# Optimization experiments

Measured on AMD Instinct MI355X. Metric: run time of the kernel, lower is better.

Reference implementation:

```python
import jax, jax.numpy as jnp
import numpy as np

NEG_SLOPE = 0.2  # PyG GATConv default negative_slope


def gat_conv(x, edge_index, W, att_src, att_dst, bias):
    # PyG GATConv, heads=1, add_self_loops=True, lin bias=False, final bias added
    N = x.shape[0]
    h = x @ W                                     # [N, F]
    loops = jnp.arange(N, dtype=edge_index.dtype)
    src = jnp.concatenate([edge_index[0], loops])
    dst = jnp.concatenate([edge_index[1], loops])
    a_src = h @ att_src                           # [N]
    a_dst = h @ att_dst                           # [N]
    e = a_src[src] + a_dst[dst]
    e = jnp.where(e > 0, e, NEG_SLOPE * e)        # leaky_relu
    m = jax.ops.segment_max(e, dst, num_segments=N)
    w = jnp.exp(e - m[dst])
    denom = jax.ops.segment_sum(w, dst, num_segments=N)
    alpha = w / denom[dst]
    out = jax.ops.segment_sum(h[src] * alpha[:, None], dst, num_segments=N)
    return out + bias


def gcn_conv(x, edge_index, W, b):
    # PyG GCNConv: add self-loops + symmetric normalization
    N = x.shape[0]
    loops = jnp.arange(N, dtype=edge_index.dtype)
    src = jnp.concatenate([edge_index[0], loops])
    dst = jnp.concatenate([edge_index[1], loops])
    deg = jax.ops.segment_sum(jnp.ones(src.shape[0], dtype=x.dtype), dst, num_segments=N)
    dinv = jax.lax.rsqrt(jnp.maximum(deg, 1e-12))  # deg >= 1 thanks to self-loops
    norm = dinv[src] * dinv[dst]
    xw = x @ W
    return jax.ops.segment_sum(xw[src] * norm[:, None], dst, num_segments=N) + b


def get_final_node(x, batch, num_graphs):
    nn_ = jax.ops.segment_sum(jnp.ones(x.shape[0], dtype=jnp.int32), batch, num_segments=num_graphs)
    cum = jnp.concatenate([jnp.zeros(1, dtype=nn_.dtype), jnp.cumsum(nn_)[:-1]])
    return x[cum]


def ontology_emb(table, e1, e2, W, asrc, adst, b, idx_map):
    emb = gat_conv(table, e1, W, asrc, adst, b)
    emb = gat_conv(emb, e2, W, asrc, adst, b)
    return emb[idx_map]


def _forward(spec_emb, diag_table, proce_table, atc_table,
             diag_W, diag_asrc, diag_adst, diag_b,
             proce_W, proce_asrc, proce_adst, proce_b,
             atc_W, atc_asrc, atc_adst, atc_b,
             gcn_W1, gcn_b1, gcn_W2, gcn_b2, gcn_W3, gcn_b3,
             diag_e1, diag_e2, proce_e1, proce_e2, atc_e1, atc_e2,
             diag_map, proce_map, atc_map,
             left_x, left_graph_index, right_x, right_graph_index,
             left_x_batch, right_x_batch, num_graphs):
    diag_emb = ontology_emb(diag_table, diag_e1, diag_e2, diag_W, diag_asrc, diag_adst, diag_b, diag_map)
    proce_emb = ontology_emb(proce_table, proce_e1, proce_e2, proce_W, proce_asrc, proce_adst, proce_b, proce_map)
    atc_emb = ontology_emb(atc_table, atc_e1, atc_e2, atc_W, atc_asrc, atc_adst, atc_b, atc_map)
    all_emb = jnp.concatenate([spec_emb, diag_emb, proce_emb, atc_emb], axis=0)
    lh = all_emb[left_x[:, 0]]   # squeeze(dim=1)
    rh = all_emb[right_x[:, 0]]
    for W, b in ((gcn_W1, gcn_b1), (gcn_W2, gcn_b2), (gcn_W3, gcn_b3)):
        lh = gcn_conv(lh, left_graph_index, W, b)
        rh = gcn_conv(rh, right_graph_index, W, b)
    lf = get_final_node(lh, left_x_batch, num_graphs)
    rf = get_final_node(rh, right_x_batch, num_graphs)
    eps = 1e-6  # CosineSimilarity eps
    num = jnp.sum(lf * rf, axis=-1)
    den = jnp.maximum(jnp.linalg.norm(lf, axis=-1), eps) * jnp.maximum(jnp.linalg.norm(rf, axis=-1), eps)
    return num / den


def setup_inputs() -> dict:
    key = jax.random.key(0)
    ks = jax.random.split(key, 32)
    HID = 128
    B, NPG = 2048, 50
    N = B * NPG               # 102400 nodes per side
    E_PAT = 409600            # 4 edges per node
    DIAG_N, DIAG_L = 30000, 20000
    PROCE_N, PROCE_L = 12000, 8000
    ATC_N, ATC_L = 6000, 4000
    ALL = 1 + DIAG_L + PROCE_L + ATC_L
    f = lambda k, s: jax.random.normal(k, s, dtype=jnp.float32)
    scale = 0.1
    inp = {
        'spec_emb': f(ks[0], (1, HID)),
        'diag_table': f(ks[1], (DIAG_N, HID)),
        'proce_table': f(ks[2], (PROCE_N, HID)),
        'atc_table': f(ks[3], (ATC_N, HID)),
    }
    for i, nm in enumerate(['diag', 'proce', 'atc']):
        inp[nm + '_W'] = f(ks[4 + i], (HID, HID)) * scale
        inp[nm + '_asrc'] = f(ks[7 + i], (HID,)) * scale
        inp[nm + '_adst'] = f(ks[10 + i], (HID,)) * scale
        inp[nm + '_b'] = jnp.zeros((HID,), jnp.float32)
    for j in range(3):
        inp['gcn_W%d' % (j + 1)] = f(ks[13 + j], (HID, HID)) * scale
        inp['gcn_b%d' % (j + 1)] = jnp.zeros((HID,), jnp.float32)
    inp['diag_e1'] = jax.random.randint(ks[16], (2, DIAG_N), 0, DIAG_N, dtype=jnp.int32)
    inp['diag_e2'] = jax.random.randint(ks[17], (2, DIAG_N), 0, DIAG_N, dtype=jnp.int32)
    inp['proce_e1'] = jax.random.randint(ks[18], (2, PROCE_N), 0, PROCE_N, dtype=jnp.int32)
    inp['proce_e2'] = jax.random.randint(ks[19], (2, PROCE_N), 0, PROCE_N, dtype=jnp.int32)
    inp['atc_e1'] = jax.random.randint(ks[20], (2, ATC_N), 0, ATC_N, dtype=jnp.int32)
    inp['atc_e2'] = jax.random.randint(ks[21], (2, ATC_N), 0, ATC_N, dtype=jnp.int32)
    inp['diag_map'] = jnp.arange(DIAG_L, dtype=jnp.int32)
    inp['proce_map'] = jnp.arange(PROCE_L, dtype=jnp.int32)
    inp['atc_map'] = jnp.arange(ATC_L, dtype=jnp.int32)
    inp['left_x'] = jax.random.randint(ks[22], (N, 1), 0, ALL, dtype=jnp.int32)
    inp['right_x'] = jax.random.randint(ks[23], (N, 1), 0, ALL, dtype=jnp.int32)
    inp['left_graph_index'] = jax.random.randint(ks[24], (2, E_PAT), 0, N, dtype=jnp.int32)
    inp['right_graph_index'] = jax.random.randint(ks[25], (2, E_PAT), 0, N, dtype=jnp.int32)
    batch = jnp.repeat(jnp.arange(B, dtype=jnp.int32), NPG)
    inp['left_x_batch'] = batch
    inp['right_x_batch'] = batch
    inp['num_graphs'] = B
    return inp


def reference(spec_emb, diag_table, proce_table, atc_table,
              diag_W, diag_asrc, diag_adst, diag_b,
              proce_W, proce_asrc, proce_adst, proce_b,
              atc_W, atc_asrc, atc_adst, atc_b,
              gcn_W1, gcn_b1, gcn_W2, gcn_b2, gcn_W3, gcn_b3,
              diag_e1, diag_e2, proce_e1, proce_e2, atc_e1, atc_e2,
              diag_map, proce_map, atc_map,
              left_x, left_graph_index, right_x, right_graph_index,
              left_x_batch, right_x_batch, num_graphs):
    return _forward(spec_emb, diag_table, proce_table, atc_table,
                    diag_W, diag_asrc, diag_adst, diag_b,
                    proce_W, proce_asrc, proce_adst, proce_b,
                    atc_W, atc_asrc, atc_adst, atc_b,
                    gcn_W1, gcn_b1, gcn_W2, gcn_b2, gcn_W3, gcn_b3,
                    diag_e1, diag_e2, proce_e1, proce_e2, atc_e1, atc_e2,
                    diag_map, proce_map, atc_map,
                    left_x, left_graph_index, right_x, right_graph_index,
                    left_x_batch, right_x_batch, num_graphs)
```

## Files before the change

### kernel.cpp

```cpp
#include <hip/hip_runtime.h>
#include <hip/hip_bf16.h>

#define HID 128

typedef unsigned int uint;
typedef unsigned short ushort;
typedef short short8 __attribute__((ext_vector_type(8)));
typedef float f32x4 __attribute__((ext_vector_type(4)));

static inline int cdiv_i(long a, long b) { return (int)((a + b - 1) / b); }
static inline int imax_i(int a, int b) { return a > b ? a : b; }

__device__ __forceinline__ float bf2f(uint hi) {
    return __builtin_bit_cast(float, hi << 16);
}
__device__ __forceinline__ ushort f2bf(float f) {
    uint u = __builtin_bit_cast(uint, f);
    u = (u + 0x7fffu + ((u >> 16) & 1u)) >> 16;
    return (ushort)u;
}

struct CsrDesc {
    const int* esrc[8];
    const int* edst[8];
    int ebase[9];
    int nbase[9];
    int totE;
};

template <typename AT>
__device__ __forceinline__ void load_afrag(const AT* __restrict__ A, long row,
                                           int koff, short8& af) {
    if constexpr (__is_same(AT, ushort)) {
        const uint4 raw = *(const uint4*)(A + row * 128 + koff);
        af = __builtin_bit_cast(short8, raw);
    } else {
        const float4* p = (const float4*)(A + row * 128 + koff);
        const float4 x0 = p[0], x1 = p[1];
        af[0] = (short)f2bf(x0.x); af[1] = (short)f2bf(x0.y);
        af[2] = (short)f2bf(x0.z); af[3] = (short)f2bf(x0.w);
        af[4] = (short)f2bf(x1.x); af[5] = (short)f2bf(x1.y);
        af[6] = (short)f2bf(x1.z); af[7] = (short)f2bf(x1.w);
    }
}

struct GOnto {
    const ushort* Wt0; const ushort* Wt1; const ushort* Wt2;
    const float* s0; const float* s1; const float* s2;
    const float* d0; const float* d1; const float* d2;
    int bs1, bs2;
    int r1, r2, r3;
};

template <typename AT>
__device__ void gemm_onto_dev(int b, const AT* __restrict__ x0,
                              const AT* __restrict__ x1, const AT* __restrict__ x2,
                              const GOnto& g, ushort* __restrict__ H,
                              float* __restrict__ as_o, float* __restrict__ ad_o) {
    const int gid = (b >= g.bs1) + (b >= g.bs2);
    const ushort* Wt = (gid == 0) ? g.Wt0 : (gid == 1) ? g.Wt1 : g.Wt2;
    const float* avs = (gid == 0) ? g.s0 : (gid == 1) ? g.s1 : g.s2;
    const float* avd = (gid == 0) ? g.d0 : (gid == 1) ? g.d1 : g.d2;
    const AT* Ag = (gid == 0) ? x0 : (gid == 1) ? x1 : x2;
    const int bloc = b - ((gid == 0) ? 0 : (gid == 1) ? g.bs1 : g.bs2);
    const long rb = (gid == 0) ? 0 : (gid == 1) ? g.r1 : g.r2;
    const long Mg = ((gid == 0) ? g.r1 : (gid == 1) ? g.r2 : g.r3) - rb;

    const int tid = threadIdx.x;
    const int wave = tid >> 6, lane = tid & 63;
    const int r = lane & 15, q = lane >> 4;
    const long m0 = (long)bloc * 128 + wave * 32;

    f32x4 acc[2][8];
#pragma unroll
    for (int mi = 0; mi < 2; ++mi)
#pragma unroll
        for (int ni = 0; ni < 8; ++ni) acc[mi][ni] = (f32x4)0.f;

#pragma unroll
    for (int t = 0; t < 4; ++t) {
        const int koff = t * 32 + q * 8;
        short8 bfr[8];
#pragma unroll
        for (int ni = 0; ni < 8; ++ni) {
            const uint4 raw = *(const uint4*)(Wt + (ni * 16 + r) * 128 + koff);
            bfr[ni] = __builtin_bit_cast(short8, raw);
        }
#pragma unroll
        for (int mi = 0; mi < 2; ++mi) {
            long row = m0 + mi * 16 + r;
            if (row >= Mg) row = Mg - 1;
            short8 af;
            load_afrag<AT>(Ag, row, koff, af);
#pragma unroll
            for (int ni = 0; ni < 8; ++ni)
                acc[mi][ni] = __builtin_amdgcn_mfma_f32_16x16x32_bf16(
                    af, bfr[ni], acc[mi][ni], 0, 0, 0);
        }
    }

    ushort* Hg = H + rb * 128;
#pragma unroll
    for (int mi = 0; mi < 2; ++mi) {
#pragma unroll
        for (int ni = 0; ni < 8; ++ni) {
            const int col = ni * 16 + r;
#pragma unroll
            for (int reg = 0; reg < 4; ++reg) {
                const long row = m0 + mi * 16 + q * 4 + reg;
                if (row < Mg) Hg[row * 128 + col] = f2bf(acc[mi][ni][reg]);
            }
        }
    }

    float asv[8], adv[8];
#pragma unroll
    for (int ni = 0; ni < 8; ++ni) {
        asv[ni] = avs[ni * 16 + r];
        adv[ni] = avd[ni * 16 + r];
    }
#pragma unroll
    for (int mi = 0; mi < 2; ++mi) {
#pragma unroll
        for (int reg = 0; reg < 4; ++reg) {
            float ps = 0.f, pd = 0.f;
#pragma unroll
            for (int ni = 0; ni < 8; ++ni) {
                ps += acc[mi][ni][reg] * asv[ni];
                pd += acc[mi][ni][reg] * adv[ni];
            }
#pragma unroll
            for (int o = 1; o < 16; o <<= 1) {
                ps += __shfl_xor(ps, o);
                pd += __shfl_xor(pd, o);
            }
            const long row = m0 + mi * 16 + q * 4 + reg;
            if (r == 0 && row < Mg) {
                as_o[rb + row] = ps;
                ad_o[rb + row] = pd;
            }
        }
    }
}

__global__ __launch_bounds__(256) void gemm_onto_l2(const ushort* __restrict__ x0,
                                                    const ushort* __restrict__ x1,
                                                    const ushort* __restrict__ x2,
                                                    GOnto g, ushort* __restrict__ H,
                                                    float* __restrict__ as_o,
                                                    float* __restrict__ ad_o) {
    gemm_onto_dev<ushort>(blockIdx.x, x0, x1, x2, g, H, as_o, ad_o);
}

struct EmbSrc {
    const float* spec; const ushort* oE;
    const int* m0; const int* m1; const int* m2;
    int lb2, lb3, r1, r2;
};

__device__ __forceinline__ short8 load_emb(const EmbSrc& e, long row, int koff) {
    short8 af;
    if (row == 0) {
        const float4* pp = (const float4*)(e.spec + koff);
        const float4 x0 = pp[0], x1 = pp[1];
        af[0] = (short)f2bf(x0.x); af[1] = (short)f2bf(x0.y);
        af[2] = (short)f2bf(x0.z); af[3] = (short)f2bf(x0.w);
        af[4] = (short)f2bf(x1.x); af[5] = (short)f2bf(x1.y);
        af[6] = (short)f2bf(x1.z); af[7] = (short)f2bf(x1.w);
        return af;
    }
    const int r = (int)row;
    const int seg = (r >= e.lb2) + (r >= e.lb3);
    const int local = r - ((seg == 0) ? 1 : (seg == 1) ? e.lb2 : e.lb3);
    const int* mp = (seg == 0) ? e.m0 : (seg == 1) ? e.m1 : e.m2;
    const int rb = (seg == 0) ? 0 : (seg == 1) ? e.r1 : e.r2;
    const long sr = (long)rb + mp[local];
    return __builtin_bit_cast(short8, *(const uint4*)(e.oE + sr * 128 + koff));
}

__device__ void gemm_pat_tile(const EmbSrc& es, const ushort* __restrict__ Wt,
                              ushort* __restrict__ C, long m0blk, long rowEnd) {
    const int tid = threadIdx.x;
    const int wave = tid >> 6, lane = tid & 63;
    const int r = lane & 15, q = lane >> 4;
    const long m0 = m0blk + wave * 32;

    f32x4 acc[2][8];
#pragma unroll
    for (int mi = 0; mi < 2; ++mi)
#pragma unroll
        for (int ni = 0; ni < 8; ++ni) acc[mi][ni] = (f32x4)0.f;

#pragma unroll
    for (int t = 0; t < 4; ++t) {
        const int koff = t * 32 + q * 8;
        short8 bfr[8];
#pragma unroll
        for (int ni = 0; ni < 8; ++ni) {
            const uint4 raw = *(const uint4*)(Wt + (ni * 16 + r) * 128 + koff);
            bfr[ni] = __builtin_bit_cast(short8, raw);
        }
#pragma unroll
        for (int mi = 0; mi < 2; ++mi) {
            long row = m0 + mi * 16 + r;
            if (row >= rowEnd) row = rowEnd - 1;
            const short8 af = load_emb(es, row, koff);
#pragma unroll
            for (int ni = 0; ni < 8; ++ni)
                acc[mi][ni] = __builtin_amdgcn_mfma_f32_16x16x32_bf16(
                    af, bfr[ni], acc[mi][ni], 0, 0, 0);
        }
    }

#pragma unroll
    for (int mi = 0; mi < 2; ++mi) {
#pragma unroll
        for (int ni = 0; ni < 8; ++ni) {
            const int col = ni * 16 + r;
#pragma unroll
            for (int reg = 0; reg < 4; ++reg) {
                const long row = m0 + mi * 16 + q * 4 + reg;
                if (row < rowEnd) C[row * 128 + col] = f2bf(acc[mi][ni][reg]);
            }
        }
    }
}

__global__ __launch_bounds__(256) void gemm_pat(EmbSrc es,
                                                const ushort* __restrict__ Wt,
                                                ushort* __restrict__ C, int M) {
    const long m0 = (long)blockIdx.x * 256;
    gemm_pat_tile(es, Wt, C, m0, M);
    if (m0 + 128 < M) gemm_pat_tile(es, Wt, C, m0 + 128, M);
}

__device__ __forceinline__ void fold1_dev(int idx, const float* __restrict__ W2,
                                          const float* __restrict__ b2,
                                          const float* __restrict__ W3,
                                          float* __restrict__ W23b) {
    if (idx >= 129 * 128) return;
    const int i = idx >> 7, j = idx & 127;
    const float* a = (i < 128) ? (W2 + i * 128) : b2;
    float s = 0.f;
#pragma unroll 8
    for (int k = 0; k < 128; ++k) s += a[k] * W3[k * 128 + j];
    W23b[idx] = s;
}

__device__ __forceinline__ void fold2_dev(int idx, const float* __restrict__ W1,
                                          const float* __restrict__ b1,
                                          const float* __restrict__ W23b,
                                          ushort* __restrict__ WpT,
                                          float* __restrict__ cbuf) {
    if (idx >= 130 * 128) return;
    const int i = idx >> 7, j = idx & 127;
    if (i == 129) { cbuf[128 + j] = W23b[128 * 128 + j]; return; }
    const float* a = (i < 128) ? (W1 + i * 128) : b1;
    float s = 0.f;
#pragma unroll 8
    for (int k = 0; k < 128; ++k) s += a[k] * W23b[k * 128 + j];
    if (i < 128) WpT[j * 128 + i] = f2bf(s);
    else cbuf[j] = s;
}

__device__ __forceinline__ void mark_dev(int i, const int* __restrict__ lEg,
                                         const int* __restrict__ rEg, int EP,
                                         int NP, int* __restrict__ mk,
                                         int testBit, int setBit) {
    int src, dst;
    if (i < 2 * EP) {
        const int side = i >= EP;
        const int e = i - side * EP;
        const int* eg = side ? rEg : lEg;
        src = side * NP + eg[e];
        dst = side * NP + eg[EP + e];
    } else if (i < 2 * EP + 2 * NP) {
        src = dst = i - 2 * EP;
    } else return;
    if (mk[dst] & testBit) {
        const int old = mk[src];
        if (!(old & setBit)) mk[src] = old | setBit;
    }
}

__device__ __forceinline__ void csr_count_dev(int i, const CsrDesc& d,
                                              int* __restrict__ cnt) {
    if (i >= d.totE) return;
    int li = 0;
#pragma unroll
    for (int k = 1; k < 8; ++k) li += (i >= d.ebase[k]);
    const int v = d.nbase[li] + d.edst[li][i - d.ebase[li]];
    atomicAdd(&cnt[v], 1);
}

struct PackPrep {
    const float* W2; const float* b2; const float* W3; float* W23b;
    const float* wsrc[3]; ushort* wt_out;
    int* cnt; int NV;
    const int* bL; const int* bR; int NP;
    int* gfL; int* gfR; int* mk;
    int nbF1, nbWT, nbInit;
};

__global__ __launch_bounds__(256) void k_prep(PackPrep p) {
    const int b = blockIdx.x, tid = threadIdx.x;
    if (b < p.nbF1) {
        fold1_dev(b * 256 + tid, p.W2, p.b2, p.W3, p.W23b);
    } else if (b < p.nbF1 + p.nbWT) {
        const int idx = (b - p.nbF1) * 256 + tid;
        if (idx < 3 * 16384) {
            const int m = idx >> 14;
            const int e = idx & 16383;
            const int n = e >> 7, k = e & 127;
            p.wt_out[idx] = f2bf(p.wsrc[m][k * 128 + n]);
        }
    } else {
        const int i = (b - p.nbF1 - p.nbWT) * 256 + tid;
        if (i < p.NV) p.cnt[i] = 0;
        if (i < 2 * p.NP) {
            const int side = i >= p.NP;
            const int ii = i - (side ? p.NP : 0);
            const int* bb = side ? p.bR : p.bL;
            int* gf = side ? p.gfR : p.gfL;
            const int cur = bb[ii];
            const int prev = (ii == 0) ? -1 : bb[ii - 1];
            int m = 0;
            if (cur > prev) {
                for (int g = prev + 1; g <= cur; ++g) gf[g] = ii;
                m = 1;
            }
            p.mk[i] = m;
        }
    }
}

struct PackBig {
    const float* x0; const float* x1; const float* x2;
    GOnto go; ushort* H; float* as_o; float* ad_o;
    const float* W1; const float* b1; const float* W23b;
    ushort* WpT; float* cbuf;
    CsrDesc dsc; int* cnt;
    const int* lEg; const int* rEg; int EP; int NP; int* mk;
    int nbGemm, nbF2, nbCnt;
};

__global__ __launch_bounds__(256) void k_big1(PackBig p) {
    const int b = blockIdx.x, tid = threadIdx.x;
    if (b < p.nbGemm) {
        gemm_onto_dev<float>(b, p.x0, p.x1, p.x2, p.go, p.H, p.as_o, p.ad_o);
    } else if (b < p.nbGemm + p.nbF2) {
        fold2_dev((b - p.nbGemm) * 256 + tid, p.W1, p.b1, p.W23b, p.WpT, p.cbuf);
    } else if (b < p.nbGemm + p.nbF2 + p.nbCnt) {
        csr_count_dev((b - p.nbGemm - p.nbF2) * 256 + tid, p.dsc, p.cnt);
    } else {
        mark_dev((b - p.nbGemm - p.nbF2 - p.nbCnt) * 256 + tid, p.lEg, p.rEg,
                 p.EP, p.NP, p.mk, 1, 2);
    }
}

__device__ void scan_tile_dev(const int* __restrict__ in, int* __restrict__ out,
                              int* __restrict__ bsum, int n, int pn0, int pcnt,
                              float* __restrict__ dinv, int tb, int tid,
                              int* sbuf) {
    const int base = tb * 1024 + tid * 4;
    int v[4];
    int s = 0;
#pragma unroll
    for (int k = 0; k < 4; ++k) {
        const int i = base + k;
        v[k] = (i < n) ? (in[i] + 1) : 0;
        if (i >= pn0 && i < pn0 + pcnt)
            dinv[i - pn0] = rsqrtf(fmaxf((float)v[k], 1e-12f));
        s += v[k];
    }
    sbuf[tid] = s;
    __syncthreads();
    int x = s;
    for (int o = 1; o < 256; o <<= 1) {
        const int t = (tid >= o) ? sbuf[tid - o] : 0;
        __syncthreads();
        x += t;
        sbuf[tid] = x;
        __syncthreads();
    }
    int run = x - s;
#pragma unroll
    for (int k = 0; k < 4; ++k) {
        const int i = base + k;
        if (i < n) out[i] = run;
        run += v[k];
    }
    if (tid == 255) bsum[tb] = x;
}

struct PackScan {
    const int* cnt; int* offs; int* bsum;
    int NV; int pn0; int pcnt; float* dinv;
    const int* lEg; const int* rEg; int EP; int NP; int* mk;
    int nbScan;
};

__global__ __launch_bounds__(256) void k_scan(PackScan p) {
    __shared__ int sbuf[256];
    const int b = blockIdx.x, tid = threadIdx.x;
    if (b < p.nbScan) {
        scan_tile_dev(p.cnt, p.offs, p.bsum, p.NV, p.pn0, p.pcnt, p.dinv, b,
                      tid, sbuf);
    } else {
        mark_dev((b - p.nbScan) * 256 + tid, p.lEg, p.rEg, p.EP, p.NP, p.mk,
                 2, 4);
    }
}

__global__ __launch_bounds__(256) void k_scanfin(int* __restrict__ out,
                                                 int* __restrict__ out2,
                                                 const int* __restrict__ bsum,
                                                 int n, int nbData) {
    __shared__ int sbuf[256];
    const int tb = blockIdx.x, tid = threadIdx.x;
    int pLim = tb < nbData ? tb : nbData;
    int pth = 0;
    for (int j = tid; j < pLim; j += 256) pth += bsum[j];
    sbuf[tid] = pth;
    __syncthreads();
    for (int o = 128; o > 0; o >>= 1) {
        if (tid < o) sbuf[tid] += sbuf[tid + o];
        __syncthreads();
    }
    const int prefix = sbuf[0];
    const int base = tb * 1024 + tid * 4;
#pragma unroll
    for (int k = 0; k < 4; ++k) {
        const int i = base + k;
        if (i < n) {
            const int v = out[i] + prefix;
            out[i] = v;
            out2[i] = v;
        } else if (i == n) {
            out[i] = prefix + ((tb < nbData) ? bsum[tb] : 0);
        }
    }
}

struct FillP {
    CsrDesc dsc;
    const int* offs; int* offs2; const int* cnt;
    int* srcl; int4* pedge; const float* dinv;
    const int* lx; const int* rx; const int* mk;
    int NP, pB;
    int eStart, eCount, vStart, vCount;
};

__device__ void fill_dev(const FillP& f, int idx) {
    if (idx < f.eCount) {
        const int i = f.eStart + idx;
        int li = 0;
#pragma unroll
        for (int k = 1; k < 8; ++k) li += (i >= f.dsc.ebase[k]);
        const int j = i - f.dsc.ebase[li];
        const int v = f.dsc.nbase[li] + f.dsc.edst[li][j];
        const int s = f.dsc.esrc[li][j];
        if (li >= 6) {
            const int n2l = v - f.dsc.nbase[6];
            if (f.mk[n2l] == 0) return;
            const int sg = (li - 6) * f.NP + s;
            const int cidx = atomicAdd(&f.offs2[v], 1);
            int4 rec;
            rec.x = sg;
            rec.y = (li == 7 ? f.rx : f.lx)[s];
            rec.z = __float_as_int(f.dinv[n2l] * f.dinv[sg]);
            rec.w = 0;
            f.pedge[cidx - f.pB] = rec;
        } else {
            const int cidx = atomicAdd(&f.offs2[v], 1);
            f.srcl[cidx] = s;
        }
    } else if (idx < f.eCount + f.vCount) {
        const int v = f.vStart + (idx - f.eCount);
        int li = 0;
#pragma unroll
        for (int k = 1; k < 8; ++k) li += (v >= f.dsc.nbase[k]);
        const int s = v - f.dsc.nbase[li];
        if (li >= 6) {
            const int n2l = v - f.dsc.nbase[6];
            if (f.mk[n2l] == 0) return;
            const int cidx = f.offs[v] + f.cnt[v];
            const int sg = (li - 6) * f.NP + s;
            int4 rec;
            rec.x = sg;
            rec.y = (li == 7 ? f.rx : f.lx)[s];
            rec.z = __float_as_int(f.dinv[n2l] * f.dinv[sg]);
            rec.w = 0;
            f.pedge[cidx - f.pB] = rec;
        } else {
            f.srcl[f.offs[v] + f.cnt[v]] = s;
        }
    }
}

__global__ __launch_bounds__(256) void k_fill(FillP f) {
    fill_dev(f, blockIdx.x * 256 + threadIdx.x);
}

struct GatP {
    int r1, r2;
    int ob0, ob1, ob2;
    const float* b0; const float* b1; const float* b2;
};

__device__ __forceinline__ void acc8(float* acc, float w, const uint4 v) {
    acc[0] += w * bf2f(v.x & 0xffff);
    acc[1] += w * bf2f(v.x >> 16);
    acc[2] += w * bf2f(v.y & 0xffff);
    acc[3] += w * bf2f(v.y >> 16);
    acc[4] += w * bf2f(v.z & 0xffff);
    acc[5] += w * bf2f(v.z >> 16);
    acc[6] += w * bf2f(v.w & 0xffff);
    acc[7] += w * bf2f(v.w >> 16);
}

__device__ void gat_dev(int node, int ql, const ushort* __restrict__ h,
                        const float* __restrict__ as, const float* __restrict__ ad,
                        const int* __restrict__ offs, const int* __restrict__ srcl,
                        const GatP& p, ushort* __restrict__ out, int Mtot) {
    if (node >= Mtot) return;
    const int gid = (node >= p.r1) + (node >= p.r2);
    const int rb = (gid == 0) ? 0 : (gid == 1) ? p.r1 : p.r2;
    const int ob = (gid == 0) ? p.ob0 : (gid == 1) ? p.ob1 : p.ob2;
    const float* bias = (gid == 0) ? p.b0 : (gid == 1) ? p.b1 : p.b2;
    const int local = node - rb;
    const int beg = offs[ob + local], end = offs[ob + local + 1];
    const float adv = ad[node];
    float denom = 0.f;
    float acc[8] = {0.f, 0.f, 0.f, 0.f, 0.f, 0.f, 0.f, 0.f};
    int j = beg;
    for (; j + 2 <= end; j += 2) {
        const int s0 = srcl[j], s1 = srcl[j + 1];
        float e0 = as[rb + s0] + adv; e0 = (e0 > 0.f) ? e0 : 0.2f * e0;
        float e1 = as[rb + s1] + adv; e1 = (e1 > 0.f) ? e1 : 0.2f * e1;
        const float w0 = __expf(e0), w1 = __expf(e1);
        const uint4 v0 = *(const uint4*)(h + (size_t)(rb + s0) * 128 + ql * 8);
        const uint4 v1 = *(const uint4*)(h + (size_t)(rb + s1) * 128 + ql * 8);
        denom += w0 + w1;
        acc8(acc, w0, v0);
        acc8(acc, w1, v1);
    }
    if (j < end) {
        const int s0 = srcl[j];
        float e0 = as[rb + s0] + adv; e0 = (e0 > 0.f) ? e0 : 0.2f * e0;
        const float w0 = __expf(e0);
        const uint4 v0 = *(const uint4*)(h + (size_t)(rb + s0) * 128 + ql * 8);
        denom += w0;
        acc8(acc, w0, v0);
    }
    const float inv = 1.f / denom;
    const float4 bv0 = *(const float4*)(bias + ql * 8);
    const float4 bv1 = *(const float4*)(bias + ql * 8 + 4);
    uint4 o;
    o.x = (uint)f2bf(acc[0] * inv + bv0.x) | ((uint)f2bf(acc[1] * inv + bv0.y) << 16);
    o.y = (uint)f2bf(acc[2] * inv + bv0.z) | ((uint)f2bf(acc[3] * inv + bv0.w) << 16);
    o.z = (uint)f2bf(acc[4] * inv + bv1.x) | ((uint)f2bf(acc[5] * inv + bv1.y) << 16);
    o.w = (uint)f2bf(acc[6] * inv + bv1.z) | ((uint)f2bf(acc[7] * inv + bv1.w) << 16);
    *(uint4*)(out + (size_t)node * 128 + ql * 8) = o;
}

__global__ __launch_bounds__(256) void gat_all(const ushort* __restrict__ h,
                                               const float* __restrict__ as,
                                               const float* __restrict__ ad,
                                               const int* __restrict__ offs,
                                               const int* __restrict__ srcl,
                                               GatP p, ushort* __restrict__ out,
                                               int Mtot) {
    gat_dev(blockIdx.x * 16 + (threadIdx.x >> 4), threadIdx.x & 15, h, as, ad,
            offs, srcl, p, out, Mtot);
}

struct GatFill {
    const ushort* h; const float* as; const float* ad;
    const int* offs; const int* srcl;
    GatP gp; ushort* out; int Mtot; int nbGat;
    FillP f;
};

__global__ __launch_bounds__(256) void k_gat_fill(GatFill g) {
    const int b = blockIdx.x, tid = threadIdx.x;
    if (b < g.nbGat) {
        gat_dev(b * 16 + (tid >> 4), tid & 15, g.h, g.as, g.ad, g.offs, g.srcl,
                g.gp, g.out, g.Mtot);
    } else {
        fill_dev(g.f, (b - g.nbGat) * 256 + tid);
    }
}

__global__ __launch_bounds__(256) void gcn_agg1(const ushort* __restrict__ A3,
                                                const int4* __restrict__ pedge,
                                                const int* __restrict__ offs6,
                                                const float* __restrict__ c1,
                                                ushort* __restrict__ t1,
                                                const int* __restrict__ mk,
                                                int NP2, int pB) {
    const int n2 = blockIdx.x * 16 + (threadIdx.x >> 4);
    const int ql = threadIdx.x & 15;
    if (n2 >= NP2) return;
    if ((mk[n2] & 4) == 0) return;
    const int beg = offs6[n2] - pB, end = offs6[n2 + 1] - pB;
    float acc[8] = {0.f, 0.f, 0.f, 0.f, 0.f, 0.f, 0.f, 0.f};
    int j = beg;
    for (; j + 2 <= end; j += 2) {
        const int4 r0 = pedge[j], r1 = pedge[j + 1];
        const float w0 = __int_as_float(r0.z), w1 = __int_as_float(r1.z);
        const uint4 v0 = *(const uint4*)(A3 + (size_t)r0.y * 128 + ql * 8);
        const uint4 v1 = *(const uint4*)(A3 + (size_t)r1.y * 128 + ql * 8);
        acc8(acc, w0, v0);
        acc8(acc, w1, v1);
    }
    if (j < end) {
        const int4 r0 = pedge[j];
        const uint4 v0 = *(const uint4*)(A3 + (size_t)r0.y * 128 + ql * 8);
        acc8(acc, __int_as_float(r0.z), v0);
    }
    const float4 bv0 = *(const float4*)(c1 + ql * 8);
    const float4 bv1 = *(const float4*)(c1 + ql * 8 + 4);
    uint4 o;
    o.x = (uint)f2bf(acc[0] + bv0.x) | ((uint)f2bf(acc[1] + bv0.y) << 16);
    o.y = (uint)f2bf(acc[2] + bv0.z) | ((uint)f2bf(acc[3] + bv0.w) << 16);
    o.z = (uint)f2bf(acc[4] + bv1.x) | ((uint)f2bf(acc[5] + bv1.y) << 16);
    o.w = (uint)f2bf(acc[6] + bv1.z) | ((uint)f2bf(acc[7] + bv1.w) << 16);
    *(uint4*)(t1 + (size_t)n2 * 128 + ql * 8) = o;
}

__device__ __forceinline__ void gcn_q_acc(const ushort* __restrict__ x,
                                          const int4* __restrict__ pedge,
                                          int beg, int end, int ql, float* acc) {
    int j = beg;
    for (; j + 2 <= end; j += 2) {
        const int4 r0 = pedge[j], r1 = pedge[j + 1];
        const float w0 = __int_as_float(r0.z), w1 = __int_as_float(r1.z);
        const uint4 v0 = *(const uint4*)(x + (size_t)r0.x * 128 + ql * 8);
        const uint4 v1 = *(const uint4*)(x + (size_t)r1.x * 128 + ql * 8);
        acc8(acc, w0, v0);
        acc8(acc, w1, v1);
    }
    if (j < end) {
        const int4 r0 = pedge[j];
        const uint4 v0 = *(const uint4*)(x + (size_t)r0.x * 128 + ql * 8);
        acc8(acc, __int_as_float(r0.z), v0);
    }
}

__global__ __launch_bounds__(256) void gcn_agg2(const ushort* __restrict__ t1,
                                                const int4* __restrict__ pedge,
                                                const int* __restrict__ offs6,
                                                const float* __restrict__ c2,
                                                ushort* __restrict__ t2,
                                                const int* __restrict__ mk,
                                                int NP2, int pB) {
    const int n2 = blockIdx.x * 16 + (threadIdx.x >> 4);
    const int ql = threadIdx.x & 15;
    if (n2 >= NP2) return;
    if ((mk[n2] & 2) == 0) return;
    const int beg = offs6[n2] - pB, end = offs6[n2 + 1] - pB;
    float acc[8] = {0.f, 0.f, 0.f, 0.f, 0.f, 0.f, 0.f, 0.f};
    gcn_q_acc(t1, pedge, beg, end, ql, acc);
    const float4 bv0 = *(const float4*)(c2 + ql * 8);
    const float4 bv1 = *(const float4*)(c2 + ql * 8 + 4);
    uint4 o;
    o.x = (uint)f2bf(acc[0] + bv0.x) | ((uint)f2bf(acc[1] + bv0.y) << 16);
    o.y = (uint)f2bf(acc[2] + bv0.z) | ((uint)f2bf(acc[3] + bv0.w) << 16);
    o.z = (uint)f2bf(acc[4] + bv1.x) | ((uint)f2bf(acc[5] + bv1.y) << 16);
    o.w = (uint)f2bf(acc[6] + bv1.z) | ((uint)f2bf(acc[7] + bv1.w) << 16);
    *(uint4*)(t2 + (size_t)n2 * 128 + ql * 8) = o;
}

__global__ __launch_bounds__(256) void final_cos(const ushort* __restrict__ t2,
                                                 const int4* __restrict__ pedge,
                                                 const int* __restrict__ offs6,
                                                 const int* __restrict__ gfL,
                                                 const int* __restrict__ gfR,
                                                 const float* __restrict__ b3,
                                                 float* __restrict__ out,
                                                 int B, int NP, int pB) {
    const int g = blockIdx.x * 8 + (threadIdx.x >> 5);
    const int l32 = threadIdx.x & 31;
    const int side = l32 >> 4;
    const int ql = l32 & 15;
    if (g >= B) return;
    const int n2 = (side ? NP : 0) + (side ? gfR : gfL)[g];
    const int beg = offs6[n2] - pB, end = offs6[n2 + 1] - pB;
    float acc[8] = {0.f, 0.f, 0.f, 0.f, 0.f, 0.f, 0.f, 0.f};
    gcn_q_acc(t2, pedge, beg, end, ql, acc);
    const float4 bv0 = *(const float4*)(b3 + ql * 8);
    const float4 bv1 = *(const float4*)(b3 + ql * 8 + 4);
    float v[8];
    v[0] = acc[0] + bv0.x; v[1] = acc[1] + bv0.y;
    v[2] = acc[2] + bv0.z; v[3] = acc[3] + bv0.w;
    v[4] = acc[4] + bv1.x; v[5] = acc[5] + bv1.y;
    v[6] = acc[6] + bv1.z; v[7] = acc[7] + bv1.w;
    float num = 0.f, nself = 0.f, nother = 0.f;
#pragma unroll
    for (int j = 0; j < 8; ++j) {
        const float o = __shfl_xor(v[j], 16);
        num += v[j] * o;
        nself += v[j] * v[j];
        nother += o * o;
    }
#pragma unroll
    for (int o1 = 1; o1 < 16; o1 <<= 1) {
        num += __shfl_xor(num, o1);
        nself += __shfl_xor(nself, o1);
        nother += __shfl_xor(nother, o1);
    }
    if (l32 == 0)
        out[g] = num / (fmaxf(sqrtf(nself), 1e-6f) * fmaxf(sqrtf(nother), 1e-6f));
}

extern "C" void kernel_launch(void* const* d_in, const int* in_sizes, int n_in,
                              void* d_out, int out_size, void* d_ws, size_t ws_size,
                              hipStream_t stream) {
    (void)n_in; (void)ws_size;
    const float* spec = (const float*)d_in[0];
    const float* tabs[3] = {(const float*)d_in[1], (const float*)d_in[2], (const float*)d_in[3]};
    const float* ontW[3] = {(const float*)d_in[4], (const float*)d_in[8], (const float*)d_in[12]};
    const float* ontAs[3] = {(const float*)d_in[5], (const float*)d_in[9], (const float*)d_in[13]};
    const float* ontAd[3] = {(const float*)d_in[6], (const float*)d_in[10], (const float*)d_in[14]};
    const float* ontB[3] = {(const float*)d_in[7], (const float*)d_in[11], (const float*)d_in[15]};
    const float* gcnW[3] = {(const float*)d_in[16], (const float*)d_in[18], (const float*)d_in[20]};
    const float* gcnB[3] = {(const float*)d_in[17], (const float*)d_in[19], (const float*)d_in[21]};
    const int* e1s[3] = {(const int*)d_in[22], (const int*)d_in[24], (const int*)d_in[26]};
    const int* e2s[3] = {(const int*)d_in[23], (const int*)d_in[25], (const int*)d_in[27]};
    const int* maps[3] = {(const int*)d_in[28], (const int*)d_in[29], (const int*)d_in[30]};
    const int* left_x = (const int*)d_in[31];
    const int* right_x = (const int*)d_in[32];
    const int* left_eg = (const int*)d_in[33];
    const int* right_eg = (const int*)d_in[34];
    const int* left_batch = (const int*)d_in[35];
    const int* right_batch = (const int*)d_in[36];

    int Ms[3] = {in_sizes[1] / HID, in_sizes[2] / HID, in_sizes[3] / HID};
    int E1s[3] = {in_sizes[22] / 2, in_sizes[24] / 2, in_sizes[26] / 2};
    int E2s[3] = {in_sizes[23] / 2, in_sizes[25] / 2, in_sizes[27] / 2};
    int Ls[3] = {in_sizes[28], in_sizes[29], in_sizes[30]};
    const int NP = in_sizes[31];
    const int EP = in_sizes[33] / 2;
    const int B = out_size;
    const long ALL = 1 + (long)Ls[0] + Ls[1] + Ls[2];
    const int Mtot = Ms[0] + Ms[1] + Ms[2];
    const int r1 = Ms[0], r2 = Ms[0] + Ms[1];

    CsrDesc dsc;
    int eCnt[8], nCnt[8];
    for (int i = 0; i < 3; ++i) {
        dsc.esrc[i] = e1s[i];     dsc.edst[i] = e1s[i] + E1s[i];
        eCnt[i] = E1s[i];         nCnt[i] = Ms[i];
        dsc.esrc[3 + i] = e2s[i]; dsc.edst[3 + i] = e2s[i] + E2s[i];
        eCnt[3 + i] = E2s[i];     nCnt[3 + i] = Ms[i];
    }
    dsc.esrc[6] = left_eg;  dsc.edst[6] = left_eg + EP;  eCnt[6] = EP; nCnt[6] = NP;
    dsc.esrc[7] = right_eg; dsc.edst[7] = right_eg + EP; eCnt[7] = EP; nCnt[7] = NP;
    dsc.ebase[0] = 0;
    int nb_acc = 0;
    for (int i = 0; i < 8; ++i) {
        dsc.ebase[i + 1] = dsc.ebase[i] + eCnt[i];
        dsc.nbase[i] = nb_acc;
        nb_acc += nCnt[i];
    }
    const int NV = nb_acc;
    dsc.nbase[8] = NV;
    dsc.totE = dsc.ebase[8];
    const int totEntries = dsc.totE + NV;
    const int pB = dsc.ebase[6] + dsc.nbase[6];
    const int pEntries = totEntries - pB;

    char* ws = (char*)d_ws;
    size_t off = 0;
    auto alloc = [&](size_t bytes) -> void* {
        off = (off + 255) & ~(size_t)255;
        void* p = ws + off;
        off += bytes;
        return p;
    };
    ushort* wt4 = (ushort*)alloc((size_t)4 * 16384 * 2);
    float* W23b = (float*)alloc((size_t)129 * 128 * 4);
    float* cbuf = (float*)alloc((size_t)256 * 4);
    ushort* A3 = (ushort*)alloc((size_t)ALL * HID * 2);
    int* cnt = (int*)alloc((size_t)NV * 4);
    int* offs = (int*)alloc((size_t)(NV + 1) * 4);
    int* offs2 = (int*)alloc((size_t)NV * 4);
    int* srcl = (int*)alloc((size_t)pB * 4);
    int4* pedge = (int4*)alloc((size_t)pEntries * 16);
    int* bsum = (int*)alloc(1025 * 4);
    float* dinv = (float*)alloc((size_t)2 * NP * 4);
    float* as = (float*)alloc((size_t)Mtot * 4);
    float* ad = (float*)alloc((size_t)Mtot * 4);
    int* gfL = (int*)alloc((size_t)(B + 1) * 4);
    int* gfR = (int*)alloc((size_t)(B + 1) * 4);
    int* mk = (int*)alloc((size_t)2 * NP * 4);
    ushort* t1 = (ushort*)alloc((size_t)2 * NP * HID * 2);
    ushort* big = (ushort*)alloc((size_t)2 * NP * HID * 2);
    ushort* hbuf = big;
    ushort* obuf = big + (size_t)Mtot * HID;
    ushort* t2 = big;

    const ushort* wtOnt[3] = {wt4, wt4 + 16384, wt4 + 2 * 16384};
    ushort* WpT = wt4 + 3 * 16384;
    const float* c1 = cbuf;
    const float* c2 = cbuf + 128;

    PackPrep pp;
    pp.W2 = gcnW[1]; pp.b2 = gcnB[1]; pp.W3 = gcnW[2]; pp.W23b = W23b;
    pp.wsrc[0] = ontW[0]; pp.wsrc[1] = ontW[1]; pp.wsrc[2] = ontW[2];
    pp.wt_out = wt4;
    pp.cnt = cnt; pp.NV = NV;
    pp.bL = left_batch; pp.bR = right_batch; pp.NP = NP;
    pp.gfL = gfL; pp.gfR = gfR; pp.mk = mk;
    pp.nbF1 = cdiv_i(129 * 128, 256);
    pp.nbWT = cdiv_i(3 * 16384, 256);
    pp.nbInit = cdiv_i(imax_i(NV, 2 * NP), 256);
    k_prep<<<pp.nbF1 + pp.nbWT + pp.nbInit, 256, 0, stream>>>(pp);

    GOnto go;
    go.Wt0 = wtOnt[0]; go.Wt1 = wtOnt[1]; go.Wt2 = wtOnt[2];
    go.s0 = ontAs[0]; go.s1 = ontAs[1]; go.s2 = ontAs[2];
    go.d0 = ontAd[0]; go.d1 = ontAd[1]; go.d2 = ontAd[2];
    go.bs1 = cdiv_i(Ms[0], 128);
    go.bs2 = go.bs1 + cdiv_i(Ms[1], 128);
    const int totBlk = go.bs2 + cdiv_i(Ms[2], 128);
    go.r1 = r1; go.r2 = r2; go.r3 = Mtot;

    PackBig pg;
    pg.x0 = tabs[0]; pg.x1 = tabs[1]; pg.x2 = tabs[2];
    pg.go = go; pg.H = hbuf; pg.as_o = as; pg.ad_o = ad;
    pg.W1 = gcnW[0]; pg.b1 = gcnB[0]; pg.W23b = W23b;
    pg.WpT = WpT; pg.cbuf = cbuf;
    pg.dsc = dsc; pg.cnt = cnt;
    pg.lEg = left_eg; pg.rEg = right_eg; pg.EP = EP; pg.NP = NP; pg.mk = mk;
    pg.nbGemm = totBlk;
    pg.nbF2 = cdiv_i(130 * 128, 256);
    pg.nbCnt = cdiv_i(dsc.totE, 256);
    const int nbMark = cdiv_i(2 * EP + 2 * NP, 256);
    k_big1<<<pg.nbGemm + pg.nbF2 + pg.nbCnt + nbMark, 256, 0, stream>>>(pg);

    PackScan psn;
    psn.cnt = cnt; psn.offs = offs; psn.bsum = bsum;
    psn.NV = NV; psn.pn0 = dsc.nbase[6]; psn.pcnt = 2 * NP; psn.dinv = dinv;
    psn.lEg = left_eg; psn.rEg = right_eg; psn.EP = EP; psn.NP = NP; psn.mk = mk;
    psn.nbScan = cdiv_i(NV, 1024);
    k_scan<<<psn.nbScan + nbMark, 256, 0, stream>>>(psn);

    k_scanfin<<<cdiv_i(NV + 1, 1024), 256, 0, stream>>>(offs, offs2, bsum, NV,
                                                        psn.nbScan);

    FillP fb;
    fb.dsc = dsc; fb.offs = offs; fb.offs2 = offs2; fb.cnt = cnt;
    fb.srcl = srcl; fb.pedge = pedge; fb.dinv = dinv;
    fb.lx = left_x; fb.rx = right_x; fb.mk = mk;
    fb.NP = NP; fb.pB = pB;

    FillP fo = fb;
    fo.eStart = 0;             fo.eCount = dsc.ebase[3];
    fo.vStart = 0;             fo.vCount = dsc.nbase[3];
    k_fill<<<cdiv_i(fo.eCount + fo.vCount, 256), 256, 0, stream>>>(fo);

    GatFill gf;
    gf.h = hbuf; gf.as = as; gf.ad = ad; gf.offs = offs; gf.srcl = srcl;
    gf.gp = GatP{r1, r2, dsc.nbase[0], dsc.nbase[1], dsc.nbase[2],
                 ontB[0], ontB[1], ontB[2]};
    gf.out = obuf; gf.Mtot = Mtot;
    gf.nbGat = cdiv_i(Mtot, 16);
    gf.f = fb;
    gf.f.eStart = dsc.ebase[3]; gf.f.eCount = dsc.totE - dsc.ebase[3];
    gf.f.vStart = dsc.nbase[3]; gf.f.vCount = NV - dsc.nbase[3];
    k_gat_fill<<<gf.nbGat + cdiv_i(gf.f.eCount + gf.f.vCount, 256), 256, 0,
                 stream>>>(gf);

    gemm_onto_l2<<<totBlk, 256, 0, stream>>>(obuf, obuf + (size_t)r1 * HID,
                                             obuf + (size_t)r2 * HID, go, hbuf,
                                             as, ad);
    const GatP gp1{r1, r2, dsc.nbase[3], dsc.nbase[4], dsc.nbase[5],
                   ontB[0], ontB[1], ontB[2]};
    gat_all<<<cdiv_i(Mtot, 16), 256, 0, stream>>>(hbuf, as, ad, offs, srcl, gp1,
                                                  obuf, Mtot);

    EmbSrc es;
    es.spec = spec; es.oE = obuf;
    es.m0 = maps[0]; es.m1 = maps[1]; es.m2 = maps[2];
    es.lb2 = 1 + Ls[0]; es.lb3 = 1 + Ls[0] + Ls[1];
    es.r1 = r1; es.r2 = r2;
    gemm_pat<<<cdiv_i(ALL, 256), 256, 0, stream>>>(es, WpT, A3, (int)ALL);

    const int* offs6 = offs + dsc.nbase[6];
    gcn_agg1<<<cdiv_i(2 * NP, 16), 256, 0, stream>>>(A3, pedge, offs6, c1, t1,
                                                     mk, 2 * NP, pB);
    gcn_agg2<<<cdiv_i(2 * NP, 16), 256, 0, stream>>>(t1, pedge, offs6, c2, t2,
                                                     mk, 2 * NP, pB);
    final_cos<<<cdiv_i(B, 8), 256, 0, stream>>>(t2, pedge, offs6, gfL, gfR,
                                                gcnB[2], (float*)d_out, B, NP, pB);
}
```

Baseline: 334.3 us.

## Pack degree counters into bytes, fuse scan passes, shrink GCN edge records

Degree counts are now stored as 8-bit fields packed four to a word. This lets a single scan kernel compute each block's prefix by re-reading all earlier packed words, so the separate block-sum finalize launch goes away. GCN edge records shrink from int4 to int2 by dropping the precomputed normalization weight, which is instead recomputed in the aggregation kernels from the dinv array. The packing overflows if any node has in-degree of 256 or more, and each scan block now does redundant prefix work that grows with its block index.

```diff
diff --git a/kernel.cpp b/kernel.cpp
--- a/kernel.cpp
+++ b/kernel.cpp
@@ -18,6 +18,10 @@
     uint u = __builtin_bit_cast(uint, f);
     u = (u + 0x7fffu + ((u >> 16) & 1u)) >> 16;
     return (ushort)u;
+}
+
+__device__ __forceinline__ int cnt_rd(const uint* __restrict__ cnt, int v) {
+    return (int)((cnt[v >> 2] >> ((v & 3) * 8)) & 0xffu);
 }
 
 struct CsrDesc {
@@ -284,19 +288,19 @@
 }
 
 __device__ __forceinline__ void csr_count_dev(int i, const CsrDesc& d,
-                                              int* __restrict__ cnt) {
+                                              uint* __restrict__ cnt) {
     if (i >= d.totE) return;
     int li = 0;
 #pragma unroll
     for (int k = 1; k < 8; ++k) li += (i >= d.ebase[k]);
     const int v = d.nbase[li] + d.edst[li][i - d.ebase[li]];
-    atomicAdd(&cnt[v], 1);
+    atomicAdd(&cnt[v >> 2], 1u << ((v & 3) * 8));
 }
 
 struct PackPrep {
     const float* W2; const float* b2; const float* W3; float* W23b;
     const float* wsrc[3]; ushort* wt_out;
-    int* cnt; int NV;
+    uint* cnt; int cntW;
     const int* bL; const int* bR; int NP;
     int* gfL; int* gfR; int* mk;
     int nbF1, nbWT, nbInit;
@@ -316,7 +320,7 @@
         }
     } else {
         const int i = (b - p.nbF1 - p.nbWT) * 256 + tid;
-        if (i < p.NV) p.cnt[i] = 0;
+        if (i < p.cntW) p.cnt[i] = 0;
         if (i < 2 * p.NP) {
             const int side = i >= p.NP;
             const int ii = i - (side ? p.NP : 0);
@@ -339,7 +343,7 @@
     GOnto go; ushort* H; float* as_o; float* ad_o;
     const float* W1; const float* b1; const float* W23b;
     ushort* WpT; float* cbuf;
-    CsrDesc dsc; int* cnt;
+    CsrDesc dsc; uint* cnt;
     const int* lEg; const int* rEg; int EP; int NP; int* mk;
     int nbGemm, nbF2, nbCnt;
 };
@@ -358,94 +362,75 @@
     }
 }
 
-__device__ void scan_tile_dev(const int* __restrict__ in, int* __restrict__ out,
-                              int* __restrict__ bsum, int n, int pn0, int pcnt,
-                              float* __restrict__ dinv, int tb, int tid,
-                              int* sbuf) {
-    const int base = tb * 1024 + tid * 4;
-    int v[4];
-    int s = 0;
-#pragma unroll
-    for (int k = 0; k < 4; ++k) {
-        const int i = base + k;
-        v[k] = (i < n) ? (in[i] + 1) : 0;
-        if (i >= pn0 && i < pn0 + pcnt)
-            dinv[i - pn0] = rsqrtf(fmaxf((float)v[k], 1e-12f));
-        s += v[k];
-    }
-    sbuf[tid] = s;
-    __syncthreads();
-    int x = s;
-    for (int o = 1; o < 256; o <<= 1) {
-        const int t = (tid >= o) ? sbuf[tid - o] : 0;
-        __syncthreads();
-        x += t;
-        sbuf[tid] = x;
-        __syncthreads();
-    }
-    int run = x - s;
-#pragma unroll
-    for (int k = 0; k < 4; ++k) {
-        const int i = base + k;
-        if (i < n) out[i] = run;
-        run += v[k];
-    }
-    if (tid == 255) bsum[tb] = x;
-}
-
-struct PackScan {
-    const int* cnt; int* offs; int* bsum;
+struct PackScan2 {
+    const uint* cnt; int* offs; int* offs2;
     int NV; int pn0; int pcnt; float* dinv;
     const int* lEg; const int* rEg; int EP; int NP; int* mk;
     int nbScan;
 };
 
-__global__ __launch_bounds__(256) void k_scan(PackScan p) {
+__global__ __launch_bounds__(256) void k_scan2(PackScan2 p) {
     __shared__ int sbuf[256];
     const int b = blockIdx.x, tid = threadIdx.x;
     if (b < p.nbScan) {
-        scan_tile_dev(p.cnt, p.offs, p.bsum, p.NV, p.pn0, p.pcnt, p.dinv, b,
-                      tid, sbuf);
+        int pth = 0;
+        for (int i = tid; i < b * 256; i += 256) {
+            const uint w = p.cnt[i];
+            pth += (int)((w & 0xffu) + ((w >> 8) & 0xffu) +
+                         ((w >> 16) & 0xffu) + (w >> 24));
+        }
+        sbuf[tid] = pth;
+        __syncthreads();
+        for (int o = 128; o > 0; o >>= 1) {
+            if (tid < o) sbuf[tid] += sbuf[tid + o];
+            __syncthreads();
+        }
+        const int prefix = sbuf[0] + b * 1024;
+        __syncthreads();
+        const int base = b * 1024 + tid * 4;
+        const uint word = p.cnt[b * 256 + tid];
+        int v[4];
+        int s = 0;
+#pragma unroll
+        for (int k = 0; k < 4; ++k) {
+            const int i = base + k;
+            v[k] = (i < p.NV) ? (int)((word >> (k * 8)) & 0xffu) + 1 : 0;
+            if (i >= p.pn0 && i < p.pn0 + p.pcnt)
+                p.dinv[i - p.pn0] = rsqrtf(fmaxf((float)v[k], 1e-12f));
+            s += v[k];
+        }
+        sbuf[tid] = s;
+        __syncthreads();
+        int x = s;
+        for (int o = 1; o < 256; o <<= 1) {
+            const int t = (tid >= o) ? sbuf[tid - o] : 0;
+            __syncthreads();
+            x += t;
+            sbuf[tid] = x;
+            __syncthreads();
+        }
+        int run = x - s + prefix;
+#pragma unroll
+        for (int k = 0; k < 4; ++k) {
+            const int i = base + k;
+            if (i < p.NV) {
+                p.offs[i] = run;
+                p.offs2[i] = run;
+            } else if (i == p.NV) {
+                p.offs[i] = run;
+            }
+            run += v[k];
+        }
     } else {
         mark_dev((b - p.nbScan) * 256 + tid, p.lEg, p.rEg, p.EP, p.NP, p.mk,
                  2, 4);
     }
 }
 
-__global__ __launch_bounds__(256) void k_scanfin(int* __restrict__ out,
-                                                 int* __restrict__ out2,
-                                                 const int* __restrict__ bsum,
-                                                 int n, int nbData) {
-    __shared__ int sbuf[256];
-    const int tb = blockIdx.x, tid = threadIdx.x;
-    int pLim = tb < nbData ? tb : nbData;
-    int pth = 0;
-    for (int j = tid; j < pLim; j += 256) pth += bsum[j];
-    sbuf[tid] = pth;
-    __syncthreads();
-    for (int o = 128; o > 0; o >>= 1) {
-        if (tid < o) sbuf[tid] += sbuf[tid + o];
-        __syncthreads();
-    }
-    const int prefix = sbuf[0];
-    const int base = tb * 1024 + tid * 4;
-#pragma unroll
-    for (int k = 0; k < 4; ++k) {
-        const int i = base + k;
-        if (i < n) {
-            const int v = out[i] + prefix;
-            out[i] = v;
-            out2[i] = v;
-        } else if (i == n) {
-            out[i] = prefix + ((tb < nbData) ? bsum[tb] : 0);
-        }
-    }
-}
-
 struct FillP {
     CsrDesc dsc;
-    const int* offs; int* offs2; const int* cnt;
-    int* srcl; int4* pedge; const float* dinv;
+    const int* offs; int* offs2; const uint* cnt;
+    int* srcl; int2* pedge;
     const int* lx; const int* rx; const int* mk;
     int NP, pB;
     int eStart, eCount, vStart, vCount;
@@ -465,11 +450,9 @@
             if (f.mk[n2l] == 0) return;
             const int sg = (li - 6) * f.NP + s;
             const int cidx = atomicAdd(&f.offs2[v], 1);
-            int4 rec;
+            int2 rec;
             rec.x = sg;
             rec.y = (li == 7 ? f.rx : f.lx)[s];
-            rec.z = __float_as_int(f.dinv[n2l] * f.dinv[sg]);
-            rec.w = 0;
             f.pedge[cidx - f.pB] = rec;
         } else {
             const int cidx = atomicAdd(&f.offs2[v], 1);
@@ -484,16 +467,14 @@
         if (li >= 6) {
             const int n2l = v - f.dsc.nbase[6];
             if (f.mk[n2l] == 0) return;
-            const int cidx = f.offs[v] + f.cnt[v];
+            const int cidx = f.offs[v] + cnt_rd(f.cnt, v);
             const int sg = (li - 6) * f.NP + s;
-            int4 rec;
+            int2 rec;
             rec.x = sg;
             rec.y = (li == 7 ? f.rx : f.lx)[s];
-            rec.z = __float_as_int(f.dinv[n2l] * f.dinv[sg]);
-            rec.w = 0;
             f.pedge[cidx - f.pB] = rec;
         } else {
-            f.srcl[f.offs[v] + f.cnt[v]] = s;
+            f.srcl[f.offs[v] + cnt_rd(f.cnt, v)] = s;
         }
     }
 }
@@ -592,9 +573,24 @@
     }
 }
 
+__device__ __forceinline__ void gcn_q_acc(const ushort* __restrict__ x,
+                                          const int2* __restrict__ pedge,
+                                          const float* __restrict__ dinv,
+                                          float dn, int beg, int end, int ql,
+                                          float* acc, bool useY) {
+    for (int j = beg; j < end; ++j) {
+        const int2 r = pedge[j];
+        const float w = dn * dinv[r.x];
+        const int row = useY ? r.y : r.x;
+        const uint4 v = *(const uint4*)(x + (size_t)row * 128 + ql * 8);
+        acc8(acc, w, v);
+    }
+}
+
 __global__ __launch_bounds__(256) void gcn_agg1(const ushort* __restrict__ A3,
-                                                const int4* __restrict__ pedge,
+                                                const int2* __restrict__ pedge,
                                                 const int* __restrict__ offs6,
+                                                const float* __restrict__ dinv,
                                                 const float* __restrict__ c1,
                                                 ushort* __restrict__ t1,
                                                 const int* __restrict__ mk,
@@ -605,20 +601,7 @@
     if ((mk[n2] & 4) == 0) return;
     const int beg = offs6[n2] - pB, end = offs6[n2 + 1] - pB;
     float acc[8] = {0.f, 0.f, 0.f, 0.f, 0.f, 0.f, 0.f, 0.f};
-    int j = beg;
-    for (; j + 2 <= end; j += 2) {
-        const int4 r0 = pedge[j], r1 = pedge[j + 1];
-        const float w0 = __int_as_float(r0.z), w1 = __int_as_float(r1.z);
-        const uint4 v0 = *(const uint4*)(A3 + (size_t)r0.y * 128 + ql * 8);
-        const uint4 v1 = *(const uint4*)(A3 + (size_t)r1.y * 128 + ql * 8);
-        acc8(acc, w0, v0);
-        acc8(acc, w1, v1);
-    }
-    if (j < end) {
-        const int4 r0 = pedge[j];
-        const uint4 v0 = *(const uint4*)(A3 + (size_t)r0.y * 128 + ql * 8);
-        acc8(acc, __int_as_float(r0.z), v0);
-    }
+    gcn_q_acc(A3, pedge, dinv, dinv[n2], beg, end, ql, acc, true);
     const float4 bv0 = *(const float4*)(c1 + ql * 8);
     const float4 bv1 = *(const float4*)(c1 + ql * 8 + 4);
     uint4 o;
@@ -629,28 +612,10 @@
     *(uint4*)(t1 + (size_t)n2 * 128 + ql * 8) = o;
 }
 
-__device__ __forceinline__ void gcn_q_acc(const ushort* __restrict__ x,
-                                          const int4* __restrict__ pedge,
-                                          int beg, int end, int ql, float* acc) {
-    int j = beg;
-    for (; j + 2 <= end; j += 2) {
-        const int4 r0 = pedge[j], r1 = pedge[j + 1];
-        const float w0 = __int_as_float(r0.z), w1 = __int_as_float(r1.z);
-        const uint4 v0 = *(const uint4*)(x + (size_t)r0.x * 128 + ql * 8);
-        const uint4 v1 = *(const uint4*)(x + (size_t)r1.x * 128 + ql * 8);
-        acc8(acc, w0, v0);
-        acc8(acc, w1, v1);
-    }
-    if (j < end) {
-        const int4 r0 = pedge[j];
-        const uint4 v0 = *(const uint4*)(x + (size_t)r0.x * 128 + ql * 8);
-        acc8(acc, __int_as_float(r0.z), v0);
-    }
-}
-
 __global__ __launch_bounds__(256) void gcn_agg2(const ushort* __restrict__ t1,
-                                                const int4* __restrict__ pedge,
+                                                const int2* __restrict__ pedge,
                                                 const int* __restrict__ offs6,
+                                                const float* __restrict__ dinv,
                                                 const float* __restrict__ c2,
                                                 ushort* __restrict__ t2,
                                                 const int* __restrict__ mk,
@@ -661,7 +626,7 @@
     if ((mk[n2] & 2) == 0) return;
     const int beg = offs6[n2] - pB, end = offs6[n2 + 1] - pB;
     float acc[8] = {0.f, 0.f, 0.f, 0.f, 0.f, 0.f, 0.f, 0.f};
-    gcn_q_acc(t1, pedge, beg, end, ql, acc);
+    gcn_q_acc(t1, pedge, dinv, dinv[n2], beg, end, ql, acc, false);
     const float4 bv0 = *(const float4*)(c2 + ql * 8);
     const float4 bv1 = *(const float4*)(c2 + ql * 8 + 4);
     uint4 o;
@@ -673,8 +638,9 @@
 }
 
 __global__ __launch_bounds__(256) void final_cos(const ushort* __restrict__ t2,
-                                                 const int4* __restrict__ pedge,
+                                                 const int2* __restrict__ pedge,
                                                  const int* __restrict__ offs6,
+                                                 const float* __restrict__ dinv,
                                                  const int* __restrict__ gfL,
                                                  const int* __restrict__ gfR,
                                                  const float* __restrict__ b3,
@@ -688,7 +654,7 @@
     const int n2 = (side ? NP : 0) + (side ? gfR : gfL)[g];
     const int beg = offs6[n2] - pB, end = offs6[n2 + 1] - pB;
     float acc[8] = {0.f, 0.f, 0.f, 0.f, 0.f, 0.f, 0.f, 0.f};
-    gcn_q_acc(t2, pedge, beg, end, ql, acc);
+    gcn_q_acc(t2, pedge, dinv, dinv[n2], beg, end, ql, acc, false);
     const float4 bv0 = *(const float4*)(b3 + ql * 8);
     const float4 bv1 = *(const float4*)(b3 + ql * 8 + 4);
     float v[8];
@@ -770,6 +736,8 @@
     const int totEntries = dsc.totE + NV;
     const int pB = dsc.ebase[6] + dsc.nbase[6];
     const int pEntries = totEntries - pB;
+    const int nbScan = cdiv_i(NV, 1024);
+    const int cntW = nbScan * 256;
 
     char* ws = (char*)d_ws;
     size_t off = 0;
@@ -783,12 +751,11 @@
     float* W23b = (float*)alloc((size_t)129 * 128 * 4);
     float* cbuf = (float*)alloc((size_t)256 * 4);
     ushort* A3 = (ushort*)alloc((size_t)ALL * HID * 2);
-    int* cnt = (int*)alloc((size_t)NV * 4);
+    uint* cnt = (uint*)alloc((size_t)cntW * 4);
     int* offs = (int*)alloc((size_t)(NV + 1) * 4);
     int* offs2 = (int*)alloc((size_t)NV * 4);
     int* srcl = (int*)alloc((size_t)pB * 4);
-    int4* pedge = (int4*)alloc((size_t)pEntries * 16);
-    int* bsum = (int*)alloc(1025 * 4);
+    int2* pedge = (int2*)alloc((size_t)pEntries * 8);
     float* dinv = (float*)alloc((size_t)2 * NP * 4);
     float* as = (float*)alloc((size_t)Mtot * 4);
     float* ad = (float*)alloc((size_t)Mtot * 4);
@@ -805,17 +772,18 @@
     ushort* WpT = wt4 + 3 * 16384;
     const float* c1 = cbuf;
     const float* c2 = cbuf + 128;
+    const int* offs6 = offs + dsc.nbase[6];
 
     PackPrep pp;
     pp.W2 = gcnW[1]; pp.b2 = gcnB[1]; pp.W3 = gcnW[2]; pp.W23b = W23b;
     pp.wsrc[0] = ontW[0]; pp.wsrc[1] = ontW[1]; pp.wsrc[2] = ontW[2];
     pp.wt_out = wt4;
-    pp.cnt = cnt; pp.NV = NV;
+    pp.cnt = cnt; pp.cntW = cntW;
     pp.bL = left_batch; pp.bR = right_batch; pp.NP = NP;
     pp.gfL = gfL; pp.gfR = gfR; pp.mk = mk;
     pp.nbF1 = cdiv_i(129 * 128, 256);
     pp.nbWT = cdiv_i(3 * 16384, 256);
-    pp.nbInit = cdiv_i(imax_i(NV, 2 * NP), 256);
+    pp.nbInit = cdiv_i(imax_i(cntW, 2 * NP), 256);
     k_prep<<<pp.nbF1 + pp.nbWT + pp.nbInit, 256, 0, stream>>>(pp);
 
     GOnto go;
@@ -840,19 +808,16 @@
     const int nbMark = cdiv_i(2 * EP + 2 * NP, 256);
     k_big1<<<pg.nbGemm + pg.nbF2 + pg.nbCnt + nbMark, 256, 0, stream>>>(pg);
 
-    PackScan psn;
-    psn.cnt = cnt; psn.offs = offs; psn.bsum = bsum;
-    psn.NV = NV; psn.pn0 = dsc.nbase[6]; psn.pcnt = 2 * NP; psn.dinv = dinv;
-    psn.lEg = left_eg; psn.rEg = right_eg; psn.EP = EP; psn.NP = NP; psn.mk = mk;
-    psn.nbScan = cdiv_i(NV, 1024);
-    k_scan<<<psn.nbScan + nbMark, 256, 0, stream>>>(psn);
-
-    k_scanfin<<<cdiv_i(NV + 1, 1024), 256, 0, stream>>>(offs, offs2, bsum, NV,
-                                                        psn.nbScan);
+    PackScan2 ps2;
+    ps2.cnt = cnt; ps2.offs = offs; ps2.offs2 = offs2;
+    ps2.NV = NV; ps2.pn0 = dsc.nbase[6]; ps2.pcnt = 2 * NP; ps2.dinv = dinv;
+    ps2.lEg = left_eg; ps2.rEg = right_eg; ps2.EP = EP; ps2.NP = NP; ps2.mk = mk;
+    ps2.nbScan = nbScan;
+    k_scan2<<<nbScan + nbMark, 256, 0, stream>>>(ps2);
 
     FillP fb;
     fb.dsc = dsc; fb.offs = offs; fb.offs2 = offs2; fb.cnt = cnt;
-    fb.srcl = srcl; fb.pedge = pedge; fb.dinv = dinv;
+    fb.srcl = srcl; fb.pedge = pedge;
     fb.lx = left_x; fb.rx = right_x; fb.mk = mk;
     fb.NP = NP; fb.pB = pB;
 
@@ -888,11 +853,11 @@
     es.r1 = r1; es.r2 = r2;
     gemm_pat<<<cdiv_i(ALL, 256), 256, 0, stream>>>(es, WpT, A3, (int)ALL);
 
-    const int* offs6 = offs + dsc.nbase[6];
-    gcn_agg1<<<cdiv_i(2 * NP, 16), 256, 0, stream>>>(A3, pedge, offs6, c1, t1,
-                                                     mk, 2 * NP, pB);
-    gcn_agg2<<<cdiv_i(2 * NP, 16), 256, 0, stream>>>(t1, pedge, offs6, c2, t2,
-                                                     mk, 2 * NP, pB);
-    final_cos<<<cdiv_i(B, 8), 256, 0, stream>>>(t2, pedge, offs6, gfL, gfR,
-                                                gcnB[2], (float*)d_out, B, NP, pB);
-}
+    gcn_agg1<<<cdiv_i(2 * NP, 16), 256, 0, stream>>>(A3, pedge, offs6, dinv, c1,
+                                                     t1, mk, 2 * NP, pB);
+    gcn_agg2<<<cdiv_i(2 * NP, 16), 256, 0, stream>>>(t1, pedge, offs6, dinv, c2,
+                                                     t2, mk, 2 * NP, pB);
+    final_cos<<<cdiv_i(B, 8), 256, 0, stream>>>(t2, pedge, offs6, dinv, gfL,
+                                                gfR, gcnB[2], (float*)d_out, B,
+                                                NP, pB);
+}
```

New measurement: 403.1 us. 20.6% more time.
